# Kernel tuning notes

Hardware: AMD Instinct MI355X
Metric: run time of the kernel (lower is better)

Reference implementation:

```python
import jax, jax.numpy as jnp
import numpy as np

INP_DIM, OUT_DIM, MID_DIM, MID_LAYERS = 3, 1, 4, 2


def _uniform(key, shape, bound):
    return jax.random.uniform(key, shape, jnp.float32, -bound, bound)


def setup_inputs() -> dict:
    key = jax.random.key(0)
    ks = jax.random.split(key, 16)
    B, T = 4096, 1024
    bnd = 1.0 / np.sqrt(MID_DIM)  # PyTorch LSTM/Linear init bound
    d = {
        "x": jax.random.normal(ks[0], (B, T, INP_DIM), jnp.float32),
        # layer 0 LSTM (gate order i,f,g,o stacked along rows)
        "W_ih0": _uniform(ks[1], (4 * MID_DIM, INP_DIM), bnd),
        "W_hh0": _uniform(ks[2], (4 * MID_DIM, MID_DIM), bnd),
        "b_ih0": _uniform(ks[3], (4 * MID_DIM,), bnd),
        "b_hh0": _uniform(ks[4], (4 * MID_DIM,), bnd),
        # layer 1 LSTM
        "W_ih1": _uniform(ks[5], (4 * MID_DIM, MID_DIM), bnd),
        "W_hh1": _uniform(ks[6], (4 * MID_DIM, MID_DIM), bnd),
        "b_ih1": _uniform(ks[7], (4 * MID_DIM,), bnd),
        "b_hh1": _uniform(ks[8], (4 * MID_DIM,), bnd),
        "W1": _uniform(ks[9], (MID_DIM, MID_DIM), bnd),
        "b1": _uniform(ks[10], (MID_DIM,), bnd),
        "W2": _uniform(ks[11], (OUT_DIM, MID_DIM), bnd),
        "b2": _uniform(ks[12], (OUT_DIM,), bnd),
    }
    return d


def _lstm_layer(x_tbd, W_ih, W_hh, b_ih, b_hh):
    # x_tbd: [T, B, D] time-major. Precompute input contribution to all gates.
    H = W_hh.shape[1]
    xg = jnp.einsum("tbd,gd->tbg", x_tbd, W_ih) + (b_ih + b_hh)  # [T,B,4H]

    def step(carry, xg_t):
        h, c = carry
        g = xg_t + h @ W_hh.T  # [B,4H]
        i, f, gg, o = jnp.split(g, 4, axis=-1)
        i = jax.nn.sigmoid(i)
        f = jax.nn.sigmoid(f)
        gg = jnp.tanh(gg)
        o = jax.nn.sigmoid(o)
        c = f * c + i * gg
        h = o * jnp.tanh(c)
        return (h, c), h

    B = x_tbd.shape[1]
    init = (jnp.zeros((B, H), x_tbd.dtype), jnp.zeros((B, H), x_tbd.dtype))
    _, hs = jax.lax.scan(step, init, xg)
    return hs  # [T,B,H]


def reference(x, W_ih0, W_hh0, b_ih0, b_hh0, W_ih1, W_hh1, b_ih1, b_hh1, W1, b1, W2, b2):
    # x: [B,T,3] (batch_first). Run 2-layer LSTM then per-timestep MLP head.
    h = jnp.transpose(x, (1, 0, 2))  # -> [T,B,3]
    h = _lstm_layer(h, W_ih0, W_hh0, b_ih0, b_hh0)
    h = _lstm_layer(h, W_ih1, W_hh1, b_ih1, b_hh1)
    h = jnp.transpose(h, (1, 0, 2))  # -> [B,T,H]
    y = jnp.tanh(h @ W1.T + b1) @ W2.T + b2  # [B,T,1]
    return y
```

## Files before the change

### kernel.cpp

```cpp
#include <hip/hip_runtime.h>


#define T_STEPS 1024
#define BATCH   4096
#define CHUNK   16
#define NCHUNK  (T_STEPS / CHUNK)
#define RDEPTH  4

__device__ __forceinline__ float fast_exp2(float x) {
#if __has_builtin(__builtin_amdgcn_exp2f)
    return __builtin_amdgcn_exp2f(x);
#else
    return exp2f(x);
#endif
}

__device__ __forceinline__ float fast_rcp(float x) {
#if __has_builtin(__builtin_amdgcn_rcpf)
    return __builtin_amdgcn_rcpf(x);
#else
    return 1.0f / x;
#endif
}

__device__ __forceinline__ float fast_tanh(float x) {
    return 2.0f * fast_rcp(1.0f + fast_exp2(-2.88539008f * x)) - 1.0f;
}

template <int CTRL>
__device__ __forceinline__ float dpp_mov(float v) {
    int i = __builtin_bit_cast(int, v);
    i = __builtin_amdgcn_mov_dpp(i, CTRL, 0xF, 0xF, true);
    return __builtin_bit_cast(float, i);
}

#define DPP_QB0         0x00
#define DPP_QB1         0x55
#define DPP_QB2         0xAA
#define DPP_QB3         0xFF
#define DPP_ROR8        0x128
#define DPP_MIRROR      0x140
#define DPP_HALF_MIRROR 0x141

__global__ __launch_bounds__(512) void lstm_r8_kernel(
    const float* __restrict__ x,
    const float* __restrict__ W_ih0, const float* __restrict__ W_hh0,
    const float* __restrict__ b_ih0, const float* __restrict__ b_hh0,
    const float* __restrict__ W_ih1, const float* __restrict__ W_hh1,
    const float* __restrict__ b_ih1, const float* __restrict__ b_hh1,
    const float* __restrict__ W1, const float* __restrict__ b1,
    const float* __restrict__ W2, const float* __restrict__ b2,
    float* __restrict__ out)
{
    __shared__ float4 xstage[4][2][68];
    __shared__ float4 ring[4][RDEPTH][CHUNK][4];
    __shared__ int done_flag[4][RDEPTH];
    __shared__ int free_flag[4][RDEPTH];

    const int tid  = threadIdx.x;
    const int wave = tid >> 6;
    const int stg  = wave >> 2;
    const int pr   = wave & 3;
    const int lane = tid & 63;
    const int idx  = lane & 15;
    const int rho  = lane & 3;
    const int u    = (lane >> 2) & 3;
    const int r    = rho * 4 + u;
    const int ch   = lane >> 4;
    const int batch = blockIdx.x * 16 + pr * 4 + ch;

    if (tid < 4 * RDEPTH) {
        done_flag[tid >> 2][tid & 3] = 0;
        free_flag[tid >> 2][tid & 3] = 0;
    }
    __syncthreads();

    const float am = (rho == 2) ? -2.88539008f : -1.44269504f;
    const float aa = (rho == 2) ? 2.0f : 1.0f;
    const float ab = (rho == 2) ? -1.0f : 0.0f;

    if (stg == 0) {
        const float wx0 = W_ih0[r * 3 + 0];
        const float wx1 = W_ih0[r * 3 + 1];
        const float wx2 = W_ih0[r * 3 + 2];
        const float bias0 = b_ih0[r] + b_hh0[r];
        float wh0[4];
#pragma unroll
        for (int k = 0; k < 4; ++k) wh0[k] = W_hh0[r * 4 + (u ^ k)];

        float h0 = 0.f, c0 = 0.f, h0b = 0.f, h0c = 0.f, h0d = 0.f;

        const float* xrow = x + (size_t)batch * T_STEPS * 3;
        const float* p0 = xrow + idx * 3;
        xstage[pr][0][ch * 17 + idx] = make_float4(p0[0], p0[1], p0[2], 0.f);
        const float* p1 = xrow + 48 + idx * 3;
        float q0 = p1[0], q1 = p1[1], q2 = p1[2];

        volatile int* ff = &free_flag[pr][0];

        for (int c = 0; c < NCHUNK; ++c) {
            const int s = c & (RDEPTH - 1);
            if (c >= RDEPTH) {
                while (ff[s] < c - RDEPTH + 1) { __builtin_amdgcn_s_sleep(1); }
            }

            const float4* xs = &xstage[pr][c & 1][ch * 17];
            float4 xc = xs[0];
#pragma unroll
            for (int tt = 0; tt < CHUNK; ++tt) {
                float4 xn = xs[(tt < CHUNK - 1) ? tt + 1 : tt];

                float pre0 = bias0 + wx0 * xc.x + wx1 * xc.y + wx2 * xc.z
                           + wh0[0] * h0 + wh0[1] * h0b + wh0[2] * h0c + wh0[3] * h0d;
                float a0 = aa * fast_rcp(1.0f + fast_exp2(am * pre0)) + ab;
                float gi = dpp_mov<DPP_QB0>(a0);
                float gf = dpp_mov<DPP_QB1>(a0);
                float gg = dpp_mov<DPP_QB2>(a0);
                float go = dpp_mov<DPP_QB3>(a0);
                c0 = gf * c0 + gi * gg;
                h0 = go * fast_tanh(c0);
                h0b = dpp_mov<DPP_HALF_MIRROR>(h0);
                h0c = dpp_mov<DPP_ROR8>(h0);
                h0d = dpp_mov<DPP_MIRROR>(h0);

                if (rho == 0) ((float*)&ring[pr][s][tt][ch])[u] = h0;
                xc = xn;
            }
            __threadfence_block();
            if (lane == 0) done_flag[pr][s] = c + 1;

            if (c < NCHUNK - 1)
                xstage[pr][(c + 1) & 1][ch * 17 + idx] = make_float4(q0, q1, q2, 0.f);
            if (c < NCHUNK - 2) {
                const float* p = xrow + (c + 2) * 48 + idx * 3;
                q0 = p[0]; q1 = p[1]; q2 = p[2];
            }
        }
    } else {
        const float bias1 = b_ih1[r] + b_hh1[r];
        float wi1[4], wh1[4], w1p[4];
#pragma unroll
        for (int k = 0; k < 4; ++k) {
            wi1[k] = W_ih1[r * 4 + k];
            wh1[k] = W_hh1[r * 4 + (u ^ k)];
            w1p[k] = W1[u * 4 + (u ^ k)];
        }
        const float b1u = b1[u];
        const float w2u = W2[u];
        const float b2v = b2[0];

        float h1 = 0.f, c1 = 0.f, h1b = 0.f, h1c = 0.f, h1d = 0.f;
        float ysave = 0.f;
        float* op = out + (size_t)batch * T_STEPS;

        volatile int* df = &done_flag[pr][0];

        for (int c = 0; c < NCHUNK; ++c) {
            const int s = c & (RDEPTH - 1);
            while (df[s] < c + 1) { __builtin_amdgcn_s_sleep(1); }
            __threadfence_block();

            const float4* rgp = &ring[pr][s][0][ch];
            float4 h_a = rgp[0];
            float4 h_b = rgp[4];
#pragma unroll
            for (int tt = 0; tt < CHUNK; ++tt) {
                float4 h_n = rgp[4 * ((tt < CHUNK - 2) ? tt + 2 : CHUNK - 1)];

                float pre1 = bias1
                           + wi1[0] * h_a.x + wi1[1] * h_a.y
                           + wi1[2] * h_a.z + wi1[3] * h_a.w
                           + wh1[0] * h1 + wh1[1] * h1b + wh1[2] * h1c + wh1[3] * h1d;
                float a1 = aa * fast_rcp(1.0f + fast_exp2(am * pre1)) + ab;
                float gi1 = dpp_mov<DPP_QB0>(a1);
                float gf1 = dpp_mov<DPP_QB1>(a1);
                float gg1 = dpp_mov<DPP_QB2>(a1);
                float go1 = dpp_mov<DPP_QB3>(a1);
                c1 = gf1 * c1 + gi1 * gg1;
                h1 = go1 * fast_tanh(c1);
                h1b = dpp_mov<DPP_HALF_MIRROR>(h1);
                h1c = dpp_mov<DPP_ROR8>(h1);
                h1d = dpp_mov<DPP_MIRROR>(h1);

                float zp = b1u + w1p[0] * h1 + w1p[1] * h1b + w1p[2] * h1c + w1p[3] * h1d;
                float z  = fast_tanh(zp);
                float yv = w2u * z;
                float t1 = yv + dpp_mov<DPP_ROR8>(yv);
                float y  = t1 + dpp_mov<DPP_MIRROR>(t1) + b2v;

                ysave = (tt == idx) ? y : ysave;
                h_a = h_b; h_b = h_n;
            }
            if (lane == 0) free_flag[pr][s] = c + 1;
            op[c * CHUNK + idx] = ysave;
        }
    }
}

extern "C" void kernel_launch(void* const* d_in, const int* in_sizes, int n_in,
                              void* d_out, int out_size, void* d_ws, size_t ws_size,
                              hipStream_t stream) {
    const float* x     = (const float*)d_in[0];
    const float* W_ih0 = (const float*)d_in[1];
    const float* W_hh0 = (const float*)d_in[2];
    const float* b_ih0 = (const float*)d_in[3];
    const float* b_hh0 = (const float*)d_in[4];
    const float* W_ih1 = (const float*)d_in[5];
    const float* W_hh1 = (const float*)d_in[6];
    const float* b_ih1 = (const float*)d_in[7];
    const float* b_hh1 = (const float*)d_in[8];
    const float* W1    = (const float*)d_in[9];
    const float* b1    = (const float*)d_in[10];
    const float* W2    = (const float*)d_in[11];
    const float* b2    = (const float*)d_in[12];
    float* out = (float*)d_out;

    dim3 grid(BATCH / 16);
    dim3 block(512);
    lstm_r8_kernel<<<grid, block, 0, stream>>>(
        x, W_ih0, W_hh0, b_ih0, b_hh0, W_ih1, W_hh1, b_ih1, b_hh1,
        W1, b1, W2, b2, out);
}
```

Before: 246.0 us.

## Split MLP head into a third pipeline stage with its own ring buffer

Moves the regression head (Linear-tanh-Linear) off the layer-1 LSTM wavefronts into a third group of 4 waves, so each block now has 12 waves in a three-stage producer/consumer pipeline. Layer 1 writes h1 into a second shared-memory ring with done/free flags, and the head waves process a whole chunk in parallel across lanes. The aim is to shorten the serial per-timestep critical path of layer 1. The cost is extra LDS traffic, more flag synchronisation, and larger blocks that may reduce occupancy.

```diff
diff --git a/kernel.cpp b/kernel.cpp
--- a/kernel.cpp
+++ b/kernel.cpp
@@ -41,8 +41,10 @@
 #define DPP_ROR8        0x128
 #define DPP_MIRROR      0x140
 #define DPP_HALF_MIRROR 0x141
-
-__global__ __launch_bounds__(512) void lstm_r8_kernel(
+#define DPP_QSWAP2      0x4E
+#define DPP_QSWAP1      0xB1
+
+__global__ __launch_bounds__(768) void lstm_r9_kernel(
     const float* __restrict__ x,
     const float* __restrict__ W_ih0, const float* __restrict__ W_hh0,
     const float* __restrict__ b_ih0, const float* __restrict__ b_hh0,
@@ -53,9 +55,12 @@
     float* __restrict__ out)
 {
     __shared__ float4 xstage[4][2][68];
-    __shared__ float4 ring[4][RDEPTH][CHUNK][4];
-    __shared__ int done_flag[4][RDEPTH];
-    __shared__ int free_flag[4][RDEPTH];
+    __shared__ float4 ring0[4][RDEPTH][CHUNK][4];
+    __shared__ float4 ring1[4][RDEPTH][CHUNK][4];
+    __shared__ int done0[4][RDEPTH];
+    __shared__ int free0[4][RDEPTH];
+    __shared__ int done1[4][RDEPTH];
+    __shared__ int free1[4][RDEPTH];
 
     const int tid  = threadIdx.x;
     const int wave = tid >> 6;
@@ -70,8 +75,10 @@
     const int batch = blockIdx.x * 16 + pr * 4 + ch;
 
     if (tid < 4 * RDEPTH) {
-        done_flag[tid >> 2][tid & 3] = 0;
-        free_flag[tid >> 2][tid & 3] = 0;
+        done0[tid >> 2][tid & 3] = 0;
+        free0[tid >> 2][tid & 3] = 0;
+        done1[tid >> 2][tid & 3] = 0;
+        free1[tid >> 2][tid & 3] = 0;
     }
     __syncthreads();
 
@@ -96,7 +103,7 @@
         const float* p1 = xrow + 48 + idx * 3;
         float q0 = p1[0], q1 = p1[1], q2 = p1[2];
 
-        volatile int* ff = &free_flag[pr][0];
+        volatile int* ff = &free0[pr][0];
 
         for (int c = 0; c < NCHUNK; ++c) {
             const int s = c & (RDEPTH - 1);
@@ -123,11 +130,11 @@
                 h0c = dpp_mov<DPP_ROR8>(h0);
                 h0d = dpp_mov<DPP_MIRROR>(h0);
 
-                if (rho == 0) ((float*)&ring[pr][s][tt][ch])[u] = h0;
+                if (rho == 0) ((float*)&ring0[pr][s][tt][ch])[u] = h0;
                 xc = xn;
             }
             __threadfence_block();
-            if (lane == 0) done_flag[pr][s] = c + 1;
+            if (lane == 0) done0[pr][s] = c + 1;
 
             if (c < NCHUNK - 1)
                 xstage[pr][(c + 1) & 1][ch * 17 + idx] = make_float4(q0, q1, q2, 0.f);
@@ -136,31 +143,29 @@
                 q0 = p[0]; q1 = p[1]; q2 = p[2];
             }
         }
-    } else {
+    } else if (stg == 1) {
         const float bias1 = b_ih1[r] + b_hh1[r];
-        float wi1[4], wh1[4], w1p[4];
+        float wi1[4], wh1[4];
 #pragma unroll
         for (int k = 0; k < 4; ++k) {
             wi1[k] = W_ih1[r * 4 + k];
             wh1[k] = W_hh1[r * 4 + (u ^ k)];
-            w1p[k] = W1[u * 4 + (u ^ k)];
-        }
-        const float b1u = b1[u];
-        const float w2u = W2[u];
-        const float b2v = b2[0];
+        }
 
         float h1 = 0.f, c1 = 0.f, h1b = 0.f, h1c = 0.f, h1d = 0.f;
-        float ysave = 0.f;
-        float* op = out + (size_t)batch * T_STEPS;
-
-        volatile int* df = &done_flag[pr][0];
+
+        volatile int* df = &done0[pr][0];
+        volatile int* f1 = &free1[pr][0];
 
         for (int c = 0; c < NCHUNK; ++c) {
             const int s = c & (RDEPTH - 1);
             while (df[s] < c + 1) { __builtin_amdgcn_s_sleep(1); }
-            __threadfence_block();
-
-            const float4* rgp = &ring[pr][s][0][ch];
+            if (c >= RDEPTH) {
+                while (f1[s] < c - RDEPTH + 1) { __builtin_amdgcn_s_sleep(1); }
+            }
+            __threadfence_block();
+
+            const float4* rgp = &ring0[pr][s][0][ch];
             float4 h_a = rgp[0];
             float4 h_b = rgp[4];
 #pragma unroll
@@ -182,17 +187,54 @@
                 h1c = dpp_mov<DPP_ROR8>(h1);
                 h1d = dpp_mov<DPP_MIRROR>(h1);
 
-                float zp = b1u + w1p[0] * h1 + w1p[1] * h1b + w1p[2] * h1c + w1p[3] * h1d;
+                if (rho == 0) ((float*)&ring1[pr][s][tt][ch])[u] = h1;
+
+                h_a = h_b; h_b = h_n;
+            }
+            if (lane == 0) free0[pr][s] = c + 1;
+            __threadfence_block();
+            if (lane == 0) done1[pr][s] = c + 1;
+        }
+    } else {
+        const int cu  = lane & 3;
+        const int sb  = (lane >> 2) & 3;
+        const int cch = lane >> 4;
+        const int cbatch = blockIdx.x * 16 + pr * 4 + cch;
+
+        float w1r[4];
+#pragma unroll
+        for (int k = 0; k < 4; ++k) w1r[k] = W1[cu * 4 + k];
+        const float b1u = b1[cu];
+        const float w2u = W2[cu];
+        const float b2v = b2[0];
+        float* op = out + (size_t)cbatch * T_STEPS;
+
+        volatile int* d1 = &done1[pr][0];
+
+        for (int c = 0; c < NCHUNK; ++c) {
+            const int s = c & (RDEPTH - 1);
+            while (d1[s] < c + 1) { __builtin_amdgcn_s_sleep(1); }
+            __threadfence_block();
+
+            const float4* rg = &ring1[pr][s][sb][cch];
+            float yq[4];
+#pragma unroll
+            for (int it = 0; it < 4; ++it) {
+                float4 h = rg[it * 16];
+                float zp = b1u + w1r[0] * h.x + w1r[1] * h.y
+                               + w1r[2] * h.z + w1r[3] * h.w;
                 float z  = fast_tanh(zp);
                 float yv = w2u * z;
-                float t1 = yv + dpp_mov<DPP_ROR8>(yv);
-                float y  = t1 + dpp_mov<DPP_MIRROR>(t1) + b2v;
-
-                ysave = (tt == idx) ? y : ysave;
-                h_a = h_b; h_b = h_n;
-            }
-            if (lane == 0) free_flag[pr][s] = c + 1;
-            op[c * CHUNK + idx] = ysave;
+                float t1 = yv + dpp_mov<DPP_QSWAP2>(yv);
+                yq[it]   = t1 + dpp_mov<DPP_QSWAP1>(t1) + b2v;
+            }
+            if (lane == 0) free1[pr][s] = c + 1;
+
+            if (cu == 0) {
+#pragma unroll
+                for (int it = 0; it < 4; ++it)
+                    op[c * CHUNK + it * 4 + sb] = yq[it];
+            }
         }
     }
 }
@@ -216,8 +258,8 @@
     float* out = (float*)d_out;
 
     dim3 grid(BATCH / 16);
-    dim3 block(512);
-    lstm_r8_kernel<<<grid, block, 0, stream>>>(
+    dim3 block(768);
+    lstm_r9_kernel<<<grid, block, 0, stream>>>(
         x, W_ih0, W_hh0, b_ih0, b_hh0, W_ih1, W_hh1, b_ih1, b_hh1,
         W1, b1, W2, b2, out);
 }
```

Measured after the change: 249.8 us. No clear change (+1.6%).
